# Kernel tuning notes

Hardware: AMD Instinct MI355X
Metric: run time of the kernel (lower is better)

## Reference

```python
import jax, jax.numpy as jnp
import numpy as np

NUM_HEADS = 4
KEY_DIM = 64
D_MODEL = 256
OUTPUT_DIM = 256


def setup_inputs() -> dict:
    key = jax.random.key(0)
    ks = jax.random.split(key, 11)
    B, T, D = 16, 1024, D_MODEL
    HD = NUM_HEADS * KEY_DIM
    s = 0.02
    return {
        "query": jax.random.normal(ks[0], (B, T, D), jnp.float32),
        "key": jax.random.normal(ks[1], (B, T, D), jnp.float32),
        "value": jax.random.normal(ks[2], (B, T, D), jnp.float32),
        "Wq": jax.random.normal(ks[3], (D, HD), jnp.float32) * s,
        "bq": jnp.zeros((HD,), jnp.float32),
        "Wk": jax.random.normal(ks[4], (D, HD), jnp.float32) * s,
        "bk": jnp.zeros((HD,), jnp.float32),
        "Wv": jax.random.normal(ks[5], (D, KEY_DIM), jnp.float32) * s,
        "bv": jnp.zeros((KEY_DIM,), jnp.float32),
        "Wo": jax.random.normal(ks[6], (HD, OUTPUT_DIM), jnp.float32) * s,
        "bo": jnp.zeros((OUTPUT_DIM,), jnp.float32),
    }


def reference(query, key, value, Wq, bq, Wk, bk, Wv, bv, Wo, bo):
    B, Tq, _ = query.shape
    Tk = key.shape[1]
    H, Dk = NUM_HEADS, KEY_DIM
    # projections
    q = (query @ Wq + bq).reshape(B, Tq, H, Dk)  # [B,Tq,H,Dk]
    k = (key @ Wk + bk).reshape(B, Tk, H, Dk)    # [B,Tk,H,Dk]
    v = value @ Wv + bv                           # [B,Tk,Dk] shared across heads
    scale = jnp.asarray(Dk, q.dtype) ** -0.5
    # scores [B,H,Tq,Tk]
    score = jnp.einsum("bqhd,bkhd->bhqk", q, k) * scale
    attn = jax.nn.softmax(score, axis=-1)
    # broadcast-V attention: [B,H,Tq,Tk] x [B,Tk,Dk] -> [B,H,Tq,Dk]
    out = jnp.einsum("bhqk,bkd->bhqd", attn, v)
    out = out.transpose(0, 2, 1, 3).reshape(B, Tq, H * Dk)
    return out @ Wo + bo
```

## Files before the change

### kernel.cpp

```cpp
#include <hip/hip_runtime.h>
#include <hip/hip_bf16.h>


typedef __attribute__((ext_vector_type(8))) short short8;
typedef __attribute__((ext_vector_type(4))) short s16x4;
typedef __attribute__((ext_vector_type(4))) float f32x4;

__device__ __forceinline__ short f2bf(float x) {
    return __builtin_bit_cast(short, __float2bfloat16(x));
}

__device__ __forceinline__ float exp2_fast(float x) {
#if __has_builtin(__builtin_amdgcn_exp2f)
    return __builtin_amdgcn_exp2f(x);
#else
    float r; asm("v_exp_f32 %0, %1" : "=v"(r) : "v"(x)); return r;
#endif
}

__device__ __forceinline__ f32x4 mfma16(short8 a, short8 b, f32x4 c) {
    return __builtin_amdgcn_mfma_f32_16x16x32_bf16(a, b, c, 0, 0, 0);
}
__device__ __forceinline__ f32x4 mfma16k16(s16x4 a, s16x4 b, f32x4 c) {
    return __builtin_amdgcn_mfma_f32_16x16x16bf16_1k(a, b, c, 0, 0, 0);
}

__device__ __forceinline__ void gll16(const float4* gsrc, float4* ldst) {
    __builtin_amdgcn_global_load_lds(
        (const __attribute__((address_space(1))) void*)gsrc,
        (__attribute__((address_space(3))) void*)ldst, 16, 0, 0);
}

#define QSCALE 0.18033688011112042f

__global__ void prep_weights(const float* __restrict__ Wq, const float* __restrict__ Wk,
                             const float* __restrict__ Wv, const float* __restrict__ Wo,
                             short* __restrict__ WqtF, short* __restrict__ WktF,
                             short* __restrict__ WvtF, short* __restrict__ WotF) {
    int tid = blockIdx.x * 256 + threadIdx.x;
    int n = tid >> 8, k = tid & 255;
    int off = ((n >> 6) << 14) + (((n >> 4) & 3) << 12) + ((k >> 5) << 9)
            + (((k >> 3) & 3) << 7) + ((n & 15) << 3) + (k & 7);
    WqtF[off] = f2bf(Wq[k * 256 + n] * QSCALE);
    WktF[off] = f2bf(Wk[k * 256 + n]);
    WotF[off] = f2bf(Wo[k * 256 + n]);
    if (n < 64) {
        int offv = ((n >> 4) << 12) + ((k >> 5) << 9) + (((k >> 3) & 3) << 7)
                 + ((n & 15) << 3) + (k & 7);
        WvtF[offv] = f2bf(Wv[k * 64 + n]);
    }
}

__global__ __launch_bounds__(256) void proj_all(
        const float* __restrict__ query, const float* __restrict__ key_,
        const float* __restrict__ value,
        const short* __restrict__ WqtF, const short* __restrict__ WktF,
        const short* __restrict__ WvtF,
        const float* __restrict__ bq, const float* __restrict__ bk,
        const float* __restrict__ bv,
        short* __restrict__ qf, short* __restrict__ kf, short* __restrict__ vf) {
    __shared__ short At[8192];
    const int tid = threadIdx.x;
    const int lane = tid & 63, wave = tid >> 6;
    const int u = lane >> 4, r16 = lane & 15;
    const int m0 = blockIdx.x * 32;
    const int task = blockIdx.y;

    const float* A = task == 0 ? query : (task == 1 ? key_ : value);

    #pragma unroll
    for (int j = 0; j < 4; ++j) {
        int p8 = j * 8 + ((wave >> 1) << 2) + u;
        int row = ((wave & 1) << 4) + r16;
        const float* src = A + (m0 + row) * 256 + p8 * 8;
        float4 a0 = *(const float4*)src;
        float4 a1 = *(const float4*)(src + 4);
        short8 w;
        w[0] = f2bf(a0.x); w[1] = f2bf(a0.y); w[2] = f2bf(a0.z); w[3] = f2bf(a0.w);
        w[4] = f2bf(a1.x); w[5] = f2bf(a1.y); w[6] = f2bf(a1.z); w[7] = f2bf(a1.w);
        int dst = ((p8 >> 2) << 10) + ((wave & 1) << 9) + ((p8 & 3) << 7) + (r16 << 3);
        *(short8*)&At[dst] = w;
    }

    const int b = m0 >> 10, t64 = (m0 & 1023) >> 6, half = (m0 >> 5) & 1;

    if (task < 2) {
        const short* WtF = task == 0 ? WqtF : WktF;
        const float* bias = task == 0 ? bq : bk;
        const float bscale = task == 0 ? QSCALE : 1.0f;
        short* outF = task == 0 ? qf : kf;
        const short* wb = WtF + (wave << 14);

        short8 bf8[4];
        #pragma unroll
        for (int g = 0; g < 4; ++g) bf8[g] = *(const short8*)&wb[(g << 12) + lane * 8];
        __syncthreads();

        f32x4 acc[2][4] = {};
        #pragma unroll
        for (int kk = 0; kk < 8; ++kk) {
            short8 af[2], nb[4];
            #pragma unroll
            for (int f = 0; f < 2; ++f) af[f] = *(const short8*)&At[(kk << 10) + (f << 9) + lane * 8];
            if (kk < 7) {
                #pragma unroll
                for (int g = 0; g < 4; ++g) nb[g] = *(const short8*)&wb[(g << 12) + ((kk + 1) << 9) + lane * 8];
            }
            #pragma unroll
            for (int f = 0; f < 2; ++f)
                #pragma unroll
                for (int g = 0; g < 4; ++g)
                    acc[f][g] = mfma16(af[f], bf8[g], acc[f][g]);
            #pragma unroll
            for (int g = 0; g < 4; ++g) bf8[g] = nb[g];
        }

        float bvv[4];
        #pragma unroll
        for (int g = 0; g < 4; ++g) bvv[g] = bias[(wave << 6) + 16 * g + r16] * bscale;
        short* ob = outF + ((((b << 2) + wave) << 4) + t64) * 4096;
        #pragma unroll
        for (int f = 0; f < 2; ++f) {
            int fg = half * 2 + f;
            #pragma unroll
            for (int g = 0; g < 4; ++g) {
                int base = (fg << 10) + ((g >> 1) << 9)
                         + (((2 * g + (r16 >> 3)) & 3) << 7) + (r16 & 7);
                #pragma unroll
                for (int rr = 0; rr < 4; ++rr)
                    ob[base + (4 * u + rr) * 8] = f2bf(acc[f][g][rr] + bvv[g]);
            }
        }
    } else {
        const int f = wave >> 1;
        short8 bf8[2];
        #pragma unroll
        for (int z = 0; z < 2; ++z) {
            int dg = ((wave & 1) << 1) + z;
            bf8[z] = *(const short8*)&WvtF[(dg << 12) + lane * 8];
        }
        __syncthreads();

        f32x4 acc[2] = {};
        #pragma unroll
        for (int kk = 0; kk < 8; ++kk) {
            short8 af = *(const short8*)&At[(kk << 10) + (f << 9) + lane * 8];
            short8 nb[2];
            if (kk < 7) {
                #pragma unroll
                for (int z = 0; z < 2; ++z) {
                    int dg = ((wave & 1) << 1) + z;
                    nb[z] = *(const short8*)&WvtF[(dg << 12) + ((kk + 1) << 9) + lane * 8];
                }
            }
            #pragma unroll
            for (int z = 0; z < 2; ++z) acc[z] = mfma16(af, bf8[z], acc[z]);
            bf8[0] = nb[0]; bf8[1] = nb[1];
        }

        short* ob = vf + ((b << 4) + t64) * 4096;
        const int gg = half * 2 + f;
        #pragma unroll
        for (int z = 0; z < 2; ++z) {
            int dg = ((wave & 1) << 1) + z;
            float bvv = bv[16 * dg + r16];
            s16x4 o;
            #pragma unroll
            for (int rr = 0; rr < 4; ++rr) o[rr] = f2bf(acc[z][rr] + bvv);
            *(s16x4*)&ob[(dg << 10) + ((gg >> 1) << 9) + lane * 8 + ((gg & 1) << 2)] = o;
        }
    }
}

__global__ __launch_bounds__(256) void attn_kernel(const short* __restrict__ qF,
        const short* __restrict__ kF, const short* __restrict__ vF,
        short* __restrict__ aoF) {
    __shared__ float4 KV[3][1024];
    const int tid = threadIdx.x;
    const int lane = tid & 63, wave = tid >> 6;
    const int u = lane >> 4, r16 = lane & 15;

    const int lin = blockIdx.x;
    const int L = (lin & 7) * 64 + (lin >> 3);
    const int qt2 = L & 7, h = (L >> 3) & 3, b = L >> 5;

    const short* qb = qF + ((((b << 2) + h) << 4) + 2 * qt2) * 4096 + (wave << 10);
    short8 qA0 = *(const short8*)&qb[lane * 8];
    short8 qA1 = *(const short8*)&qb[512 + lane * 8];
    short8 qB0 = *(const short8*)&qb[4096 + lane * 8];
    short8 qB1 = *(const short8*)&qb[4096 + 512 + lane * 8];

    const float4* kb = (const float4*)(kF + (((b << 2) + h) << 16));
    const float4* vb = (const float4*)(vF + (b << 16));

    #define STAGE(t, buf)                                                     \
        {                                                                     \
            const float4* ks_ = kb + (t) * 512;                               \
            const float4* vs_ = vb + (t) * 512;                               \
            _Pragma("unroll")                                                 \
            for (int j_ = 0; j_ < 4; ++j_) {                                  \
                int ch_ = (wave << 2) + j_;                                   \
                if (ch_ < 8) gll16(ks_ + (ch_ << 6) + lane, &KV[buf][ch_ << 6]); \
                else gll16(vs_ + ((ch_ - 8) << 6) + lane, &KV[buf][512 + ((ch_ - 8) << 6)]); \
            }                                                                 \
        }

    STAGE(0, 0)
    STAGE(1, 1)
    asm volatile("s_waitcnt vmcnt(4)" ::: "memory");
    __builtin_amdgcn_s_barrier();

    f32x4 acc0[4] = {}, acc1[4] = {};
    f32x4 accl0 = {}, accl1 = {};
    s16x4 ones;
    { short o = (short)0x3F80; ones[0] = o; ones[1] = o; ones[2] = o; ones[3] = o; }

    #pragma unroll
    for (int kt = 0; kt < 16; ++kt) {
        const int buf = kt % 3;
        if (kt + 2 < 16) STAGE(kt + 2, (kt + 2) % 3)

        const short* Kl = (const short*)&KV[buf][0];
        const short* Vl = (const short*)&KV[buf][512];

        f32x4 s0[4], s1[4];
        __builtin_amdgcn_s_setprio(1);
        #pragma unroll
        for (int g = 0; g < 4; ++g) {
            short8 k0 = *(const short8*)&Kl[(g << 10) + lane * 8];
            short8 k1 = *(const short8*)&Kl[(g << 10) + 512 + lane * 8];
            f32x4 z0 = {}, z1 = {};
            z0 = mfma16(k0, qA0, z0);
            s0[g] = mfma16(k1, qA1, z0);
            z1 = mfma16(k0, qB0, z1);
            s1[g] = mfma16(k1, qB1, z1);
        }
        __builtin_amdgcn_s_setprio(0);

        s16x4 pk0[4], pk1[4];
        #pragma unroll
        for (int g = 0; g < 4; ++g)
            #pragma unroll
            for (int rr = 0; rr < 4; ++rr) {
                pk0[g][rr] = f2bf(exp2_fast(s0[g][rr]));
                pk1[g][rr] = f2bf(exp2_fast(s1[g][rr]));
            }

        __builtin_amdgcn_s_setprio(1);
        #pragma unroll
        for (int g = 0; g < 4; ++g) {
            accl0 = mfma16k16(ones, pk0[g], accl0);
            accl1 = mfma16k16(ones, pk1[g], accl1);
        }
        #pragma unroll
        for (int dg = 0; dg < 4; ++dg) {
            #pragma unroll
            for (int gp = 0; gp < 2; ++gp) {
                short8 v8 = *(const short8*)&Vl[(dg << 10) + (gp << 9) + lane * 8];
                s16x4 vlo = { v8[0], v8[1], v8[2], v8[3] };
                s16x4 vhi = { v8[4], v8[5], v8[6], v8[7] };
                acc0[dg] = mfma16k16(vlo, pk0[2 * gp], acc0[dg]);
                acc0[dg] = mfma16k16(vhi, pk0[2 * gp + 1], acc0[dg]);
                acc1[dg] = mfma16k16(vlo, pk1[2 * gp], acc1[dg]);
                acc1[dg] = mfma16k16(vhi, pk1[2 * gp + 1], acc1[dg]);
            }
        }
        __builtin_amdgcn_s_setprio(0);

        if (kt < 14) {
            asm volatile("s_waitcnt vmcnt(4)" ::: "memory");
            __builtin_amdgcn_s_barrier();
        } else if (kt < 15) {
            asm volatile("s_waitcnt vmcnt(0)" ::: "memory");
            __builtin_amdgcn_s_barrier();
        }
    }

    float li0 = 1.0f / accl0[0];
    float li1 = 1.0f / accl1[0];

    short* ob0 = aoF + (((b << 4) + 2 * qt2) << 14);
    #pragma unroll
    for (int dg = 0; dg < 4; ++dg) {
        int off = ((2 * h + (dg >> 1)) << 11) + (wave << 9)
                + (((2 * dg + (u >> 1)) & 3) << 7) + (r16 << 3) + ((u & 1) << 2);
        s16x4 o0, o1;
        #pragma unroll
        for (int rr = 0; rr < 4; ++rr) {
            o0[rr] = f2bf(acc0[dg][rr] * li0);
            o1[rr] = f2bf(acc1[dg][rr] * li1);
        }
        *(s16x4*)&ob0[off] = o0;
        *(s16x4*)&ob0[16384 + off] = o1;
    }
    #undef STAGE
}

__global__ __launch_bounds__(256) void ogemm(const short* __restrict__ AF,
        const short* __restrict__ WoF, const float* __restrict__ bias,
        float* __restrict__ outp) {
    __shared__ short At[8192];
    const int tid = threadIdx.x;
    const int lane = tid & 63, wave = tid >> 6;
    const int u = lane >> 4, r16 = lane & 15;
    const int m0 = blockIdx.x * 32;
    const int mtile = m0 >> 6;
    const int fh = (m0 >> 4) & 2;

    const short* ab = AF + (mtile << 14) + (fh << 9);
    #pragma unroll
    for (int j = 0; j < 4; ++j) {
        int n = j * 256 + tid;
        int kk = n >> 7, rem = n & 127;
        *(short8*)&At[n * 8] = *(const short8*)&ab[(kk << 11) + rem * 8];
    }

    const short* wb = WoF + (wave << 14);
    short8 bf8[4];
    #pragma unroll
    for (int g = 0; g < 4; ++g) bf8[g] = *(const short8*)&wb[(g << 12) + lane * 8];
    __syncthreads();

    f32x4 acc[2][4] = {};
    #pragma unroll
    for (int kk = 0; kk < 8; ++kk) {
        short8 af[2], nb[4];
        #pragma unroll
        for (int f = 0; f < 2; ++f) af[f] = *(const short8*)&At[(kk << 10) + (f << 9) + lane * 8];
        if (kk < 7) {
            #pragma unroll
            for (int g = 0; g < 4; ++g) nb[g] = *(const short8*)&wb[(g << 12) + ((kk + 1) << 9) + lane * 8];
        }
        #pragma unroll
        for (int f = 0; f < 2; ++f)
            #pragma unroll
            for (int g = 0; g < 4; ++g)
                acc[f][g] = mfma16(af[f], bf8[g], acc[f][g]);
        #pragma unroll
        for (int g = 0; g < 4; ++g) bf8[g] = nb[g];
    }

    float bvv[4];
    #pragma unroll
    for (int g = 0; g < 4; ++g) bvv[g] = bias[(wave << 6) + 16 * g + r16];
    #pragma unroll
    for (int f = 0; f < 2; ++f)
        #pragma unroll
        for (int g = 0; g < 4; ++g)
            #pragma unroll
            for (int rr = 0; rr < 4; ++rr)
                outp[(m0 + 16 * f + 4 * u + rr) * 256 + (wave << 6) + 16 * g + r16]
                    = acc[f][g][rr] + bvv[g];
}

extern "C" void kernel_launch(void* const* d_in, const int* in_sizes, int n_in,
                              void* d_out, int out_size, void* d_ws, size_t ws_size,
                              hipStream_t stream) {
    (void)in_sizes; (void)n_in; (void)out_size; (void)ws_size;
    const float* query = (const float*)d_in[0];
    const float* key_  = (const float*)d_in[1];
    const float* value = (const float*)d_in[2];
    const float* Wq = (const float*)d_in[3];
    const float* bq = (const float*)d_in[4];
    const float* Wk = (const float*)d_in[5];
    const float* bk = (const float*)d_in[6];
    const float* Wv = (const float*)d_in[7];
    const float* bv = (const float*)d_in[8];
    const float* Wo = (const float*)d_in[9];
    const float* bo = (const float*)d_in[10];
    float* outp = (float*)d_out;

    short* wsp  = (short*)d_ws;
    short* WqtF = wsp;
    short* WktF = wsp + 65536;
    short* WotF = wsp + 131072;
    short* WvtF = wsp + 196608;
    short* qf   = wsp + 212992;
    short* kf   = wsp + 4407296;
    short* vf   = wsp + 8601600;
    short* aof  = wsp + 9650176;

    hipLaunchKernelGGL(prep_weights, dim3(256), dim3(256), 0, stream,
                       Wq, Wk, Wv, Wo, WqtF, WktF, WvtF, WotF);
    hipLaunchKernelGGL(proj_all, dim3(512, 3), dim3(256), 0, stream,
                       query, key_, value, WqtF, WktF, WvtF, bq, bk, bv, qf, kf, vf);
    hipLaunchKernelGGL(attn_kernel, dim3(512), dim3(256), 0, stream, qf, kf, vf, aof);
    hipLaunchKernelGGL(ogemm, dim3(512), dim3(256), 0, stream, aof, WotF, bo, outp);
}
```

Measured before the change: 62.47 us.

## Fuse attention with output projection in one all-heads-per-block kernel

Attention and the output GEMM are merged into one kernel. Each 512-thread block covers all four heads for a 64-row query tile, so one shared V tile serves every head and the attention output stays in LDS for the Wo multiply, never passing through global memory. This removes the intermediate global round trip and one kernel launch, but the grid shrinks to 256 larger blocks with a 32-step pipeline. The prep_weights index mapping is also swapped so consecutive threads read contiguous columns of the weight matrices.

```diff
diff --git a/kernel.cpp b/kernel.cpp
--- a/kernel.cpp
+++ b/kernel.cpp
@@ -38,7 +38,7 @@
                              short* __restrict__ WqtF, short* __restrict__ WktF,
                              short* __restrict__ WvtF, short* __restrict__ WotF) {
     int tid = blockIdx.x * 256 + threadIdx.x;
-    int n = tid >> 8, k = tid & 255;
+    int k = tid >> 8, n = tid & 255;
     int off = ((n >> 6) << 14) + (((n >> 4) & 3) << 12) + ((k >> 5) << 9)
             + (((k >> 3) & 3) << 7) + ((n & 15) << 3) + (k & 7);
     WqtF[off] = f2bf(Wq[k * 256 + n] * QSCALE);
@@ -172,185 +172,171 @@
     }
 }
 
-__global__ __launch_bounds__(256) void attn_kernel(const short* __restrict__ qF,
+__global__ __launch_bounds__(512, 2) void attn_og(const short* __restrict__ qF,
         const short* __restrict__ kF, const short* __restrict__ vF,
-        short* __restrict__ aoF) {
-    __shared__ float4 KV[3][1024];
+        const short* __restrict__ WoF, const float* __restrict__ bo,
+        float* __restrict__ outp) {
+    __shared__ float4 KV3[3840];
     const int tid = threadIdx.x;
     const int lane = tid & 63, wave = tid >> 6;
     const int u = lane >> 4, r16 = lane & 15;
-
-    const int lin = blockIdx.x;
-    const int L = (lin & 7) * 64 + (lin >> 3);
-    const int qt2 = L & 7, h = (L >> 3) & 3, b = L >> 5;
-
-    const short* qb = qF + ((((b << 2) + h) << 4) + 2 * qt2) * 4096 + (wave << 10);
-    short8 qA0 = *(const short8*)&qb[lane * 8];
-    short8 qA1 = *(const short8*)&qb[512 + lane * 8];
-    short8 qB0 = *(const short8*)&qb[4096 + lane * 8];
-    short8 qB1 = *(const short8*)&qb[4096 + 512 + lane * 8];
-
-    const float4* kb = (const float4*)(kF + (((b << 2) + h) << 16));
-    const float4* vb = (const float4*)(vF + (b << 16));
-
-    #define STAGE(t, buf)                                                     \
-        {                                                                     \
-            const float4* ks_ = kb + (t) * 512;                               \
-            const float4* vs_ = vb + (t) * 512;                               \
-            _Pragma("unroll")                                                 \
-            for (int j_ = 0; j_ < 4; ++j_) {                                  \
-                int ch_ = (wave << 2) + j_;                                   \
-                if (ch_ < 8) gll16(ks_ + (ch_ << 6) + lane, &KV[buf][ch_ << 6]); \
-                else gll16(vs_ + ((ch_ - 8) << 6) + lane, &KV[buf][512 + ((ch_ - 8) << 6)]); \
-            }                                                                 \
-        }
-
-    STAGE(0, 0)
-    STAGE(1, 1)
-    asm volatile("s_waitcnt vmcnt(4)" ::: "memory");
+    const int h = wave & 3, qh = wave >> 2;
+
+    const int L = (blockIdx.x & 7) * 32 + (blockIdx.x >> 3);
+    const int b = L >> 4, qt = L & 15;
+
+    const short* qb = qF + (((b << 2) + h) << 16) + (qt << 12);
+    short8 qfr[2][2];
+    #pragma unroll
+    for (int f = 0; f < 2; ++f)
+        #pragma unroll
+        for (int c = 0; c < 2; ++c)
+            qfr[f][c] = *(const short8*)&qb[((2 * qh + f) << 10) + (c << 9) + lane * 8];
+
+    #define STAGE(t, bufp)                                                          \
+        {                                                                           \
+            _Pragma("unroll")                                                       \
+            for (int j_ = 0; j_ < 3; ++j_) {                                        \
+                int ch_ = wave + 8 * j_;                                            \
+                if (ch_ < 20) {                                                     \
+                    const float4* src_;                                             \
+                    if (ch_ < 16)                                                   \
+                        src_ = (const float4*)kF + (((b << 2) + (ch_ >> 2)) * 8192) \
+                             + (t) * 256 + ((ch_ & 3) << 6) + lane;                 \
+                    else                                                            \
+                        src_ = (const float4*)vF + (b * 8192) + ((t) >> 1) * 512    \
+                             + ((ch_ - 16) << 7) + (((t) & 1) << 6) + lane;         \
+                    gll16(src_, (bufp) + (ch_ << 6));                               \
+                }                                                                   \
+            }                                                                       \
+        }
+
+    float4* bc = KV3;
+    float4* bn = KV3 + 1280;
+    float4* bs = KV3 + 2560;
+
+    STAGE(0, bc)
+    STAGE(1, bn)
+    asm volatile("s_waitcnt vmcnt(0)" ::: "memory");
     __builtin_amdgcn_s_barrier();
 
-    f32x4 acc0[4] = {}, acc1[4] = {};
-    f32x4 accl0 = {}, accl1 = {};
+    f32x4 acc[2][4] = {};
+    f32x4 accl[2] = {};
     s16x4 ones;
     { short o = (short)0x3F80; ones[0] = o; ones[1] = o; ones[2] = o; ones[3] = o; }
 
-    #pragma unroll
-    for (int kt = 0; kt < 16; ++kt) {
-        const int buf = kt % 3;
-        if (kt + 2 < 16) STAGE(kt + 2, (kt + 2) % 3)
-
-        const short* Kl = (const short*)&KV[buf][0];
-        const short* Vl = (const short*)&KV[buf][512];
-
-        f32x4 s0[4], s1[4];
+    for (int kt = 0; kt < 32; ++kt) {
+        if (kt < 30) STAGE(kt + 2, bs)
+
+        const short* Kh = (const short*)bc + (h << 11);
+        const short* Vb = (const short*)bc + 8192;
+
+        short8 kf8[4];
+        #pragma unroll
+        for (int g = 0; g < 2; ++g)
+            #pragma unroll
+            for (int c = 0; c < 2; ++c)
+                kf8[g * 2 + c] = *(const short8*)&Kh[(g << 10) + (c << 9) + lane * 8];
+
+        f32x4 s[2][2];
         __builtin_amdgcn_s_setprio(1);
         #pragma unroll
-        for (int g = 0; g < 4; ++g) {
-            short8 k0 = *(const short8*)&Kl[(g << 10) + lane * 8];
-            short8 k1 = *(const short8*)&Kl[(g << 10) + 512 + lane * 8];
-            f32x4 z0 = {}, z1 = {};
-            z0 = mfma16(k0, qA0, z0);
-            s0[g] = mfma16(k1, qA1, z0);
-            z1 = mfma16(k0, qB0, z1);
-            s1[g] = mfma16(k1, qB1, z1);
-        }
+        for (int f = 0; f < 2; ++f)
+            #pragma unroll
+            for (int g = 0; g < 2; ++g) {
+                f32x4 z = {};
+                z = mfma16(kf8[2 * g], qfr[f][0], z);
+                s[f][g] = mfma16(kf8[2 * g + 1], qfr[f][1], z);
+            }
         __builtin_amdgcn_s_setprio(0);
 
-        s16x4 pk0[4], pk1[4];
-        #pragma unroll
-        for (int g = 0; g < 4; ++g)
-            #pragma unroll
-            for (int rr = 0; rr < 4; ++rr) {
-                pk0[g][rr] = f2bf(exp2_fast(s0[g][rr]));
-                pk1[g][rr] = f2bf(exp2_fast(s1[g][rr]));
-            }
+        s16x4 pk[2][2];
+        #pragma unroll
+        for (int f = 0; f < 2; ++f)
+            #pragma unroll
+            for (int g = 0; g < 2; ++g)
+                #pragma unroll
+                for (int rr = 0; rr < 4; ++rr)
+                    pk[f][g][rr] = f2bf(exp2_fast(s[f][g][rr]));
 
         __builtin_amdgcn_s_setprio(1);
         #pragma unroll
-        for (int g = 0; g < 4; ++g) {
-            accl0 = mfma16k16(ones, pk0[g], accl0);
-            accl1 = mfma16k16(ones, pk1[g], accl1);
-        }
+        for (int f = 0; f < 2; ++f)
+            #pragma unroll
+            for (int g = 0; g < 2; ++g)
+                accl[f] = mfma16k16(ones, pk[f][g], accl[f]);
         #pragma unroll
         for (int dg = 0; dg < 4; ++dg) {
-            #pragma unroll
-            for (int gp = 0; gp < 2; ++gp) {
-                short8 v8 = *(const short8*)&Vl[(dg << 10) + (gp << 9) + lane * 8];
-                s16x4 vlo = { v8[0], v8[1], v8[2], v8[3] };
-                s16x4 vhi = { v8[4], v8[5], v8[6], v8[7] };
-                acc0[dg] = mfma16k16(vlo, pk0[2 * gp], acc0[dg]);
-                acc0[dg] = mfma16k16(vhi, pk0[2 * gp + 1], acc0[dg]);
-                acc1[dg] = mfma16k16(vlo, pk1[2 * gp], acc1[dg]);
-                acc1[dg] = mfma16k16(vhi, pk1[2 * gp + 1], acc1[dg]);
+            short8 v8 = *(const short8*)&Vb[(dg << 9) + lane * 8];
+            s16x4 vlo = { v8[0], v8[1], v8[2], v8[3] };
+            s16x4 vhi = { v8[4], v8[5], v8[6], v8[7] };
+            #pragma unroll
+            for (int f = 0; f < 2; ++f) {
+                acc[f][dg] = mfma16k16(vlo, pk[f][0], acc[f][dg]);
+                acc[f][dg] = mfma16k16(vhi, pk[f][1], acc[f][dg]);
             }
         }
         __builtin_amdgcn_s_setprio(0);
 
-        if (kt < 14) {
-            asm volatile("s_waitcnt vmcnt(4)" ::: "memory");
+        if (kt < 30) {
+            if (wave < 4) asm volatile("s_waitcnt vmcnt(3)" ::: "memory");
+            else          asm volatile("s_waitcnt vmcnt(2)" ::: "memory");
             __builtin_amdgcn_s_barrier();
-        } else if (kt < 15) {
+        } else if (kt == 30) {
             asm volatile("s_waitcnt vmcnt(0)" ::: "memory");
             __builtin_amdgcn_s_barrier();
         }
-    }
-
-    float li0 = 1.0f / accl0[0];
-    float li1 = 1.0f / accl1[0];
-
-    short* ob0 = aoF + (((b << 4) + 2 * qt2) << 14);
-    #pragma unroll
-    for (int dg = 0; dg < 4; ++dg) {
-        int off = ((2 * h + (dg >> 1)) << 11) + (wave << 9)
-                + (((2 * dg + (u >> 1)) & 3) << 7) + (r16 << 3) + ((u & 1) << 2);
-        s16x4 o0, o1;
-        #pragma unroll
-        for (int rr = 0; rr < 4; ++rr) {
-            o0[rr] = f2bf(acc0[dg][rr] * li0);
-            o1[rr] = f2bf(acc1[dg][rr] * li1);
-        }
-        *(s16x4*)&ob0[off] = o0;
-        *(s16x4*)&ob0[16384 + off] = o1;
+        float4* t_ = bc; bc = bn; bn = bs; bs = t_;
     }
     #undef STAGE
-}
-
-__global__ __launch_bounds__(256) void ogemm(const short* __restrict__ AF,
-        const short* __restrict__ WoF, const float* __restrict__ bias,
-        float* __restrict__ outp) {
-    __shared__ short At[8192];
-    const int tid = threadIdx.x;
-    const int lane = tid & 63, wave = tid >> 6;
-    const int u = lane >> 4, r16 = lane & 15;
-    const int m0 = blockIdx.x * 32;
-    const int mtile = m0 >> 6;
-    const int fh = (m0 >> 4) & 2;
-
-    const short* ab = AF + (mtile << 14) + (fh << 9);
-    #pragma unroll
-    for (int j = 0; j < 4; ++j) {
-        int n = j * 256 + tid;
-        int kk = n >> 7, rem = n & 127;
-        *(short8*)&At[n * 8] = *(const short8*)&ab[(kk << 11) + rem * 8];
-    }
-
-    const short* wb = WoF + (wave << 14);
-    short8 bf8[4];
-    #pragma unroll
-    for (int g = 0; g < 4; ++g) bf8[g] = *(const short8*)&wb[(g << 12) + lane * 8];
+
     __syncthreads();
 
-    f32x4 acc[2][4] = {};
+    short* At = (short*)KV3;
+    float linv[2] = { 1.0f / accl[0][0], 1.0f / accl[1][0] };
+    #pragma unroll
+    for (int f = 0; f < 2; ++f)
+        #pragma unroll
+        for (int dg = 0; dg < 4; ++dg) {
+            s16x4 o;
+            #pragma unroll
+            for (int rr = 0; rr < 4; ++rr) o[rr] = f2bf(acc[f][dg][rr] * linv[f]);
+            int kk = 2 * h + (dg >> 1);
+            int fq = 2 * qh + f;
+            int u2 = 2 * (dg & 1) + (u >> 1);
+            int off = (kk << 11) + (fq << 9) + ((u2 << 4) + r16) * 8 + ((u & 1) << 2);
+            *(s16x4*)&At[off] = o;
+        }
+    __syncthreads();
+
+    const short* wb = WoF + ((wave >> 1) << 14) + ((wave & 1) << 13);
+    f32x4 acc2[4][2] = {};
     #pragma unroll
     for (int kk = 0; kk < 8; ++kk) {
-        short8 af[2], nb[4];
-        #pragma unroll
-        for (int f = 0; f < 2; ++f) af[f] = *(const short8*)&At[(kk << 10) + (f << 9) + lane * 8];
-        if (kk < 7) {
-            #pragma unroll
-            for (int g = 0; g < 4; ++g) nb[g] = *(const short8*)&wb[(g << 12) + ((kk + 1) << 9) + lane * 8];
-        }
-        #pragma unroll
-        for (int f = 0; f < 2; ++f)
-            #pragma unroll
-            for (int g = 0; g < 4; ++g)
-                acc[f][g] = mfma16(af[f], bf8[g], acc[f][g]);
-        #pragma unroll
-        for (int g = 0; g < 4; ++g) bf8[g] = nb[g];
-    }
-
-    float bvv[4];
-    #pragma unroll
-    for (int g = 0; g < 4; ++g) bvv[g] = bias[(wave << 6) + 16 * g + r16];
-    #pragma unroll
-    for (int f = 0; f < 2; ++f)
-        #pragma unroll
-        for (int g = 0; g < 4; ++g)
+        short8 af[4], bf2[2];
+        #pragma unroll
+        for (int fq = 0; fq < 4; ++fq) af[fq] = *(const short8*)&At[(kk << 11) + (fq << 9) + lane * 8];
+        #pragma unroll
+        for (int gg = 0; gg < 2; ++gg) bf2[gg] = *(const short8*)&wb[(gg << 12) + (kk << 9) + lane * 8];
+        #pragma unroll
+        for (int fq = 0; fq < 4; ++fq)
+            #pragma unroll
+            for (int gg = 0; gg < 2; ++gg)
+                acc2[fq][gg] = mfma16(af[fq], bf2[gg], acc2[fq][gg]);
+    }
+
+    const int m0 = L << 6;
+    float bvv[2];
+    #pragma unroll
+    for (int gg = 0; gg < 2; ++gg) bvv[gg] = bo[(wave << 5) + (gg << 4) + r16];
+    #pragma unroll
+    for (int fq = 0; fq < 4; ++fq)
+        #pragma unroll
+        for (int gg = 0; gg < 2; ++gg)
             #pragma unroll
             for (int rr = 0; rr < 4; ++rr)
-                outp[(m0 + 16 * f + 4 * u + rr) * 256 + (wave << 6) + 16 * g + r16]
-                    = acc[f][g][rr] + bvv[g];
+                outp[(m0 + 16 * fq + 4 * u + rr) * 256 + (wave << 5) + (gg << 4) + r16]
+                    = acc2[fq][gg][rr] + bvv[gg];
 }
 
 extern "C" void kernel_launch(void* const* d_in, const int* in_sizes, int n_in,
@@ -378,12 +364,11 @@
     short* qf   = wsp + 212992;
     short* kf   = wsp + 4407296;
     short* vf   = wsp + 8601600;
-    short* aof  = wsp + 9650176;
 
     hipLaunchKernelGGL(prep_weights, dim3(256), dim3(256), 0, stream,
                        Wq, Wk, Wv, Wo, WqtF, WktF, WvtF, WotF);
     hipLaunchKernelGGL(proj_all, dim3(512, 3), dim3(256), 0, stream,
                        query, key_, value, WqtF, WktF, WvtF, bq, bk, bv, qf, kf, vf);
-    hipLaunchKernelGGL(attn_kernel, dim3(512), dim3(256), 0, stream, qf, kf, vf, aof);
-    hipLaunchKernelGGL(ogemm, dim3(512), dim3(256), 0, stream, aof, WotF, bo, outp);
-}
+    hipLaunchKernelGGL(attn_og, dim3(256), dim3(512), 0, stream,
+                       qf, kf, vf, WotF, bo, outp);
+}
```

After: 61.88 us. About the same (-0.9%).
